# Optimization experiments

Measured on AMD Instinct MI355X. Metric: run time of the kernel, lower is better.

Reference implementation:

```python
import jax, jax.numpy as jnp
import numpy as np

N_CLASS = 85
BLANK = N_CLASS - 1  # blank_index = n_class - 1
ALPHA = 0.05
B, T, D = 4096, 96, 64


def setup_inputs() -> dict:
    key = jax.random.key(0)
    k1, k2, k3, k4 = jax.random.split(key, 4)
    preds = jax.random.normal(k1, (B, T, N_CLASS), dtype=jnp.float32)
    features = jax.random.normal(k2, (B, T, D), dtype=jnp.float32)
    labels = jax.random.randint(k3, (B, T), 0, N_CLASS, dtype=jnp.int32)
    centers = jax.random.normal(k4, (N_CLASS, D), dtype=jnp.float32) * 0.01
    return {"preds": preds, "features": features, "labels": labels, "centers": centers}


def _char_mask(pred_labels):
    # CTC collapse: keep non-blank positions that are the last of a repeat run.
    is_char = pred_labels != BLANK
    rep = pred_labels[:, :-1] == pred_labels[:, 1:]          # [B, T-1]
    tail = pred_labels[:, :1] > BLANK                         # always False (as in source)
    char_rep = jnp.concatenate([rep, tail], axis=1)           # [B, T]
    return is_char & jnp.logical_not(char_rep)


def reference(preds, features, labels, centers):
    # preds:    [B, T, n_class] softmax/logits -> argmax decode
    # features: [B, T, feat_dims]
    # labels:   [B, T] int, char label aligned to each timestep
    pred_labels = jnp.argmax(preds, axis=-1)                  # [B, T]
    mask = _char_mask(pred_labels).astype(features.dtype)     # [B, T] ragged-as-mask

    centers_batch = centers[labels]                           # gather -> [B, T, D]
    diff = centers_batch - features                           # [B, T, D]

    # tf.nn.l2_loss = sum(x^2)/2, restricted to valid char positions
    loss = 0.5 * jnp.sum(mask * jnp.sum(diff * diff, axis=-1))

    # unique_with_counts analog: per-class counts of valid char positions
    labels_flat = labels.reshape(-1)
    mask_flat = mask.reshape(-1)
    counts = jax.ops.segment_sum(mask_flat, labels_flat, num_segments=N_CLASS)  # [n_class]
    appear = counts[labels]                                   # [B, T]

    # alpha * diff / (1 + appear_times), zeroed outside char positions
    delta = ALPHA * diff * (mask / (1.0 + appear))[..., None]  # [B, T, D]

    # scatter_nd: centers.assign_sub(scatter of per-char deltas)
    upd = jax.ops.segment_sum(delta.reshape(-1, D), labels_flat, num_segments=N_CLASS)
    new_centers = centers - upd                               # [n_class, D]
    return loss, new_centers
```

## Files before the change

### kernel.cpp

```cpp
#include <hip/hip_runtime.h>
#include <cstdint>

#define BB     4096
#define TT     96
#define NC     85
#define BLANKC 84
#define DD     64
#define ALPHA  0.05f
#define BT     (BB * TT)
#define SLICE_F (NC * 17)
#define NF4    (TT * NC / 4)

template<int C0, int C1>
__device__ inline void scanR(const float* __restrict__ row, float& bv, int& bc) {
    bv = row[C0]; bc = C0;
#pragma unroll
    for (int c = C0 + 1; c < C1; ++c) {
        float v = row[c];
        if (v > bv) { bv = v; bc = c; }
    }
}

__global__ __launch_bounds__(512) void k_amask(const float4* __restrict__ p4,
                                               const int* __restrict__ labels,
                                               unsigned* __restrict__ labm,
                                               int* __restrict__ hpartT,
                                               float* __restrict__ out) {
    __shared__ float rows[TT * NC];
    __shared__ float sv[4 * TT];
    __shared__ int   sc[4 * TT];
    __shared__ int   pls[TT];
    __shared__ int   h[NC];
    int tid = threadIdx.x;
    int b   = blockIdx.x;
    if (tid < NC) h[tid] = 0;
    if (b == 0 && tid == 480) out[0] = 0.f;

    const float4* src = p4 + (size_t)b * NF4;
    float4* r4 = (float4*)rows;
    float4 v[4];
#pragma unroll
    for (int k = 0; k < 4; ++k)
        v[k] = src[min(tid + k * 512, NF4 - 1)];
#pragma unroll
    for (int k = 0; k < 4; ++k) {
        int i = tid + k * 512;
        if (i < NF4) r4[i] = v[k];
    }
    __syncthreads();

    int q = tid >> 7, r = tid & 127;
    if (r < TT) {
        const float* row = rows + r * NC;
        float bv; int bc;
        switch (q) {
            case 0:  scanR< 0, 22>(row, bv, bc); break;
            case 1:  scanR<22, 43>(row, bv, bc); break;
            case 2:  scanR<43, 64>(row, bv, bc); break;
            default: scanR<64, 85>(row, bv, bc); break;
        }
        sv[q * TT + r] = bv; sc[q * TT + r] = bc;
    }
    __syncthreads();
    if (tid < TT) {
        float bv = sv[tid]; int bc = sc[tid];
#pragma unroll
        for (int qq = 1; qq < 4; ++qq) {
            float v2 = sv[qq * TT + tid];
            int   c2 = sc[qq * TT + tid];
            if (v2 > bv) { bv = v2; bc = c2; }
        }
        pls[tid] = bc;
    }
    __syncthreads();
    if (tid < TT) {
        int p = pls[tid];
        int m = (p != BLANKC) && (tid == TT - 1 || p != pls[tid + 1]);
        int lab = labels[b * TT + tid];
        labm[b * TT + tid] = (unsigned)lab | ((unsigned)m << 31);
        atomicAdd(&h[lab], m);
    }
    __syncthreads();
    if (tid < NC) hpartT[tid * BB + b] = h[tid];
}

__global__ __launch_bounds__(512) void k_main(const float* __restrict__ feat,
                                              const unsigned* __restrict__ labm,
                                              float* __restrict__ updp,
                                              float* __restrict__ lossp, int nb) {
    __shared__ float sl[8 * SLICE_F];
    __shared__ float lred[8];
    int tid = threadIdx.x;
    for (int i = tid; i < 8 * SLICE_F; i += 512) sl[i] = 0.f;
    __syncthreads();

    int lane = tid & 63;
    int w    = tid >> 6;
    int dq   = w & 3;
    int wg   = w >> 2;
    int sub  = lane >> 4;
    int l16  = lane & 15;
    float* slice = sl + w * SLICE_F;

    int ppc    = BT / (nb * 2);
    int p0     = (blockIdx.x * 2 + wg) * ppc;
    int nsteps = ppc / 4;

    float lsum = 0.f;
    uint4 lmv = *(const uint4*)(labm + p0);
    float f   = feat[(size_t)(p0 + sub) * DD + dq * 16 + l16];

    for (int s = 0; s < nsteps; ++s) {
        uint4 lv = lmv; float fc = f;
        if (s + 1 < nsteps) {
            int pn = p0 + (s + 1) * 4;
            lmv = *(const uint4*)(labm + pn);
            f   = feat[(size_t)(pn + sub) * DD + dq * 16 + l16];
        }
        unsigned a0 = lv.x & 0x7fffffffu, a1 = lv.y & 0x7fffffffu,
                 a2 = lv.z & 0x7fffffffu, a3 = lv.w & 0x7fffffffu;
        bool dup = (a0 == a1) | (a0 == a2) | (a0 == a3) |
                   (a1 == a2) | (a1 == a3) | (a2 == a3);
        unsigned lw = (sub & 2) ? ((sub & 1) ? lv.w : lv.z)
                                : ((sub & 1) ? lv.y : lv.x);
        float m = (float)(lw >> 31);
        int  la = (int)(lw & 0x7fffffffu);
        float c = m * fc;
        lsum = fmaf(c, fc, lsum);
        int a = la * 17 + l16;
        if (!dup) slice[a] += c;
        else      atomicAdd(&slice[a], c);
    }
    __syncthreads();

    float* myp = updp + (size_t)blockIdx.x * (NC * DD);
    for (int i = tid; i < NC * DD; i += 512) {
        int r = i >> 6, d = i & 63;
        int qq = d >> 4, d16 = d & 15;
        myp[i] = sl[qq * SLICE_F + r * 17 + d16] +
                 sl[(qq + 4) * SLICE_F + r * 17 + d16];
    }
#pragma unroll
    for (int off = 32; off; off >>= 1) lsum += __shfl_xor(lsum, off);
    if (lane == 0) lred[w] = lsum;
    __syncthreads();
    if (tid == 0) {
        float s = 0.f;
#pragma unroll
        for (int ww = 0; ww < 8; ++ww) s += lred[ww];
        lossp[blockIdx.x] = s;
    }
}

__global__ __launch_bounds__(256) void k_reduce(const float* __restrict__ updp,
                                                const float* __restrict__ lossp,
                                                const float* __restrict__ centers,
                                                const int* __restrict__ hpartT,
                                                float* __restrict__ out, int nb) {
    __shared__ float sred[256];
    __shared__ float sr[4];
    __shared__ int   scnt;
    int tid = threadIdx.x;
    int bid = blockIdx.x;
    if (bid < NC * 4) {
        int j = bid >> 2, q = bid & 3;
        int cs = 0;
        for (int t = tid; t < BB; t += 256) cs += hpartT[j * BB + t];
#pragma unroll
        for (int off = 32; off; off >>= 1) cs += __shfl_xor(cs, off);
        int lane = tid & 63, wv = tid >> 6;
        if (lane == 0) ((int*)sred)[wv] = cs;
        __syncthreads();
        if (tid == 0)
            scnt = ((int*)sred)[0] + ((int*)sred)[1] +
                   ((int*)sred)[2] + ((int*)sred)[3];
        __syncthreads();
        float cnt = (float)scnt;
        int i = tid & 15;
        int c16 = tid >> 4;
        int per = nb >> 4;
        int col = j * DD + q * 16 + i;
        float s = 0.f;
        for (int b = c16 * per; b < (c16 + 1) * per; ++b)
            s += updp[(size_t)b * (NC * DD) + col];
        sred[tid] = s;
        __syncthreads();
        if (tid < 16) {
            float F = 0.f;
#pragma unroll
            for (int cc = 0; cc < 16; ++cc) F += sred[cc * 16 + i];
            float c   = centers[col];
            float scale = ALPHA / (1.f + cnt);
            out[1 + col] = c - scale * (cnt * c - F);
            float lp = cnt * c * c - 2.f * c * F;
#pragma unroll
            for (int off = 8; off; off >>= 1) lp += __shfl_xor(lp, off);
            if (i == 0) atomicAdd(&out[0], 0.5f * lp);
        }
    } else {
        float s = 0.f;
        for (int t = tid; t < nb; t += 256) s += lossp[t];
#pragma unroll
        for (int off = 32; off; off >>= 1) s += __shfl_xor(s, off);
        int lane = tid & 63, wv = tid >> 6;
        if (lane == 0) sr[wv] = s;
        __syncthreads();
        if (tid == 0) atomicAdd(&out[0], 0.5f * (sr[0] + sr[1] + sr[2] + sr[3]));
    }
}

extern "C" void kernel_launch(void* const* d_in, const int* in_sizes, int n_in,
                              void* d_out, int out_size, void* d_ws, size_t ws_size,
                              hipStream_t stream) {
    const float* preds    = (const float*)d_in[0];
    const float* features = (const float*)d_in[1];
    const int*   labels   = (const int*)d_in[2];
    const float* centers  = (const float*)d_in[3];
    float* out = (float*)d_out;

    char* ws = (char*)d_ws;
    unsigned* labm = (unsigned*)ws;
    int* hpartT    = (int*)(ws + 4 * (size_t)BT);
    size_t off0 = 4 * (size_t)BT + (size_t)NC * BB * 4 + 512;

    int nb = 768;
    while (nb > 16 && off0 + (size_t)nb * 4 + 512 +
                      (size_t)nb * NC * DD * 4 > ws_size)
        nb >>= 1;
    float* lossp = (float*)(ws + off0);
    float* updp  = (float*)(ws + off0 + (size_t)nb * 4 + 512);

    k_amask<<<BB, 512, 0, stream>>>((const float4*)preds, labels, labm,
                                    hpartT, out);
    k_main<<<nb, 512, 0, stream>>>(features, labm, updp, lossp, nb);
    k_reduce<<<NC * 4 + 1, 256, 0, stream>>>(updp, lossp, centers, hpartT,
                                             out, nb);
}
```

Baseline: 88.53 us.

## Fuse argmax-mask and feature accumulation into one kernel over 512 blocks

Merges the argmax/CTC-mask kernel and the per-class feature accumulation kernel into a single kernel. Each of 512 blocks processes 8 batch rows, prefetching the next row's preds while computing the current one, then accumulates masked features into a shared per-class array. This removes the intermediate labm buffer round trip and one kernel launch. It shrinks the partial-histogram reduction from 4096 to 512 entries. In exchange it uses much more shared memory per block (about 57 KB), which limits occupancy, and adds several barriers per row.

```diff
diff --git a/kernel.cpp b/kernel.cpp
--- a/kernel.cpp
+++ b/kernel.cpp
@@ -8,8 +8,10 @@
 #define DD     64
 #define ALPHA  0.05f
 #define BT     (BB * TT)
-#define SLICE_F (NC * 17)
 #define NF4    (TT * NC / 4)
+#define NBLK   512
+#define RPB    (BB / NBLK)
+#define FSTR   73
 
 template<int C0, int C1>
 __device__ inline void scanR(const float* __restrict__ row, float& bv, int& bc) {
@@ -21,125 +23,131 @@
     }
 }
 
-__global__ __launch_bounds__(512) void k_amask(const float4* __restrict__ p4,
-                                               const int* __restrict__ labels,
-                                               unsigned* __restrict__ labm,
-                                               int* __restrict__ hpartT,
-                                               float* __restrict__ out) {
+__global__ __launch_bounds__(512, 4) void k_fused(const float4* __restrict__ p4,
+                                                  const int* __restrict__ labels,
+                                                  const float* __restrict__ feat,
+                                                  float* __restrict__ updp,
+                                                  int* __restrict__ hpartT,
+                                                  float* __restrict__ lossp,
+                                                  float* __restrict__ out) {
     __shared__ float rows[TT * NC];
+    __shared__ float Farr[NC * FSTR];
     __shared__ float sv[4 * TT];
     __shared__ int   sc[4 * TT];
-    __shared__ int   pls[TT];
+    __shared__ unsigned lab_ls[TT];
+    __shared__ int   dupflag[12];
     __shared__ int   h[NC];
-    int tid = threadIdx.x;
-    int b   = blockIdx.x;
-    if (tid < NC) h[tid] = 0;
-    if (b == 0 && tid == 480) out[0] = 0.f;
-
-    const float4* src = p4 + (size_t)b * NF4;
-    float4* r4 = (float4*)rows;
-    float4 v[4];
-#pragma unroll
-    for (int k = 0; k < 4; ++k)
-        v[k] = src[min(tid + k * 512, NF4 - 1)];
-#pragma unroll
-    for (int k = 0; k < 4; ++k) {
-        int i = tid + k * 512;
-        if (i < NF4) r4[i] = v[k];
-    }
-    __syncthreads();
-
-    int q = tid >> 7, r = tid & 127;
-    if (r < TT) {
-        const float* row = rows + r * NC;
-        float bv; int bc;
-        switch (q) {
-            case 0:  scanR< 0, 22>(row, bv, bc); break;
-            case 1:  scanR<22, 43>(row, bv, bc); break;
-            case 2:  scanR<43, 64>(row, bv, bc); break;
-            default: scanR<64, 85>(row, bv, bc); break;
-        }
-        sv[q * TT + r] = bv; sc[q * TT + r] = bc;
-    }
-    __syncthreads();
-    if (tid < TT) {
-        float bv = sv[tid]; int bc = sc[tid];
-#pragma unroll
-        for (int qq = 1; qq < 4; ++qq) {
-            float v2 = sv[qq * TT + tid];
-            int   c2 = sc[qq * TT + tid];
-            if (v2 > bv) { bv = v2; bc = c2; }
-        }
-        pls[tid] = bc;
-    }
-    __syncthreads();
-    if (tid < TT) {
-        int p = pls[tid];
-        int m = (p != BLANKC) && (tid == TT - 1 || p != pls[tid + 1]);
-        int lab = labels[b * TT + tid];
-        labm[b * TT + tid] = (unsigned)lab | ((unsigned)m << 31);
-        atomicAdd(&h[lab], m);
-    }
-    __syncthreads();
-    if (tid < NC) hpartT[tid * BB + b] = h[tid];
-}
-
-__global__ __launch_bounds__(512) void k_main(const float* __restrict__ feat,
-                                              const unsigned* __restrict__ labm,
-                                              float* __restrict__ updp,
-                                              float* __restrict__ lossp, int nb) {
-    __shared__ float sl[8 * SLICE_F];
     __shared__ float lred[8];
-    int tid = threadIdx.x;
-    for (int i = tid; i < 8 * SLICE_F; i += 512) sl[i] = 0.f;
-    __syncthreads();
-
+
+    int tid  = threadIdx.x;
+    int blk  = blockIdx.x;
     int lane = tid & 63;
     int w    = tid >> 6;
-    int dq   = w & 3;
-    int wg   = w >> 2;
-    int sub  = lane >> 4;
-    int l16  = lane & 15;
-    float* slice = sl + w * SLICE_F;
-
-    int ppc    = BT / (nb * 2);
-    int p0     = (blockIdx.x * 2 + wg) * ppc;
-    int nsteps = ppc / 4;
-
+    int sub  = lane >> 3;
+    int l8   = lane & 7;
+    int dim  = (w << 3) | l8;
+
+    for (int i = tid; i < NC * FSTR; i += 512) Farr[i] = 0.f;
+    if (tid < NC) h[tid] = 0;
+    if (blk == 0 && tid == 500) out[0] = 0.f;
+
+    int row0 = blk * RPB;
+    const float4* s0 = p4 + (size_t)row0 * NF4;
+    float4 v0 = s0[tid];
+    float4 v1 = s0[tid + 512];
+    float4 v2 = s0[tid + 1024];
+    float4 v3 = s0[tid + 1536 < NF4 ? tid + 1536 : NF4 - 1];
+    int lcur = (tid < TT) ? labels[row0 * TT + tid] : 0;
     float lsum = 0.f;
-    uint4 lmv = *(const uint4*)(labm + p0);
-    float f   = feat[(size_t)(p0 + sub) * DD + dq * 16 + l16];
-
-    for (int s = 0; s < nsteps; ++s) {
-        uint4 lv = lmv; float fc = f;
-        if (s + 1 < nsteps) {
-            int pn = p0 + (s + 1) * 4;
-            lmv = *(const uint4*)(labm + pn);
-            f   = feat[(size_t)(pn + sub) * DD + dq * 16 + l16];
-        }
-        unsigned a0 = lv.x & 0x7fffffffu, a1 = lv.y & 0x7fffffffu,
-                 a2 = lv.z & 0x7fffffffu, a3 = lv.w & 0x7fffffffu;
-        bool dup = (a0 == a1) | (a0 == a2) | (a0 == a3) |
-                   (a1 == a2) | (a1 == a3) | (a2 == a3);
-        unsigned lw = (sub & 2) ? ((sub & 1) ? lv.w : lv.z)
-                                : ((sub & 1) ? lv.y : lv.x);
-        float m = (float)(lw >> 31);
-        int  la = (int)(lw & 0x7fffffffu);
-        float c = m * fc;
-        lsum = fmaf(c, fc, lsum);
-        int a = la * 17 + l16;
-        if (!dup) slice[a] += c;
-        else      atomicAdd(&slice[a], c);
+
+    for (int r8 = 0; r8 < RPB; ++r8) {
+        int row = row0 + r8;
+        __syncthreads();
+        float4* r4 = (float4*)rows;
+        r4[tid]        = v0;
+        r4[tid + 512]  = v1;
+        r4[tid + 1024] = v2;
+        if (tid + 1536 < NF4) r4[tid + 1536] = v3;
+        if (tid < TT) lab_ls[tid] = (unsigned)lcur;
+        int lnext = 0;
+        if (r8 + 1 < RPB) {
+            const float4* sn = p4 + (size_t)(row + 1) * NF4;
+            v0 = sn[tid];
+            v1 = sn[tid + 512];
+            v2 = sn[tid + 1024];
+            v3 = sn[tid + 1536 < NF4 ? tid + 1536 : NF4 - 1];
+            if (tid < TT) lnext = labels[(row + 1) * TT + tid];
+        }
+        __syncthreads();
+        {
+            int q = tid >> 7, r = tid & 127;
+            if (r < TT) {
+                const float* rw = rows + r * NC;
+                float bv; int bc;
+                switch (q) {
+                    case 0:  scanR< 0, 22>(rw, bv, bc); break;
+                    case 1:  scanR<22, 43>(rw, bv, bc); break;
+                    case 2:  scanR<43, 64>(rw, bv, bc); break;
+                    default: scanR<64, 85>(rw, bv, bc); break;
+                }
+                sv[q * TT + r] = bv; sc[q * TT + r] = bc;
+            }
+            if (tid < 12) {
+                int l[8];
+#pragma unroll
+                for (int k = 0; k < 8; ++k) l[k] = (int)lab_ls[tid * 8 + k];
+                int d = 0;
+#pragma unroll
+                for (int a = 0; a < 8; ++a)
+#pragma unroll
+                    for (int b2 = a + 1; b2 < 8; ++b2) d |= (l[a] == l[b2]);
+                dupflag[tid] = d;
+            }
+        }
+        __syncthreads();
+        if (tid < TT) {
+            int t1 = (tid + 1 < TT) ? tid + 1 : tid;
+            float bv = sv[tid];  int bc = sc[tid];
+            float bw = sv[t1];   int bd = sc[t1];
+#pragma unroll
+            for (int q = 1; q < 4; ++q) {
+                float a = sv[q * TT + tid]; int c = sc[q * TT + tid];
+                if (a > bv) { bv = a; bc = c; }
+                float a1 = sv[q * TT + t1]; int c1 = sc[q * TT + t1];
+                if (a1 > bw) { bw = a1; bd = c1; }
+            }
+            int m = (bc != BLANKC) && (tid == TT - 1 || bc != bd);
+            lab_ls[tid] = (unsigned)lcur | ((unsigned)m << 31);
+            atomicAdd(&h[lcur], m);
+            lcur = lnext;
+        }
+        __syncthreads();
+        {
+            const float* fb = feat + (size_t)row * TT * DD;
+            int dfl[12];
+#pragma unroll
+            for (int k = 0; k < 12; ++k) dfl[k] = dupflag[k];
+            float f = fb[sub * DD + dim];
+#pragma unroll
+            for (int s = 0; s < 12; ++s) {
+                float fc = f;
+                if (s < 11) f = fb[((s + 1) * 8 + sub) * DD + dim];
+                unsigned lw = lab_ls[s * 8 + sub];
+                float m = (float)(lw >> 31);
+                int  la = (int)(lw & 0x7fffffffu);
+                float c = m * fc;
+                lsum = fmaf(c, fc, lsum);
+                int a = la * FSTR + dim;
+                if (dfl[s]) atomicAdd(&Farr[a], c);
+                else        Farr[a] += c;
+            }
+        }
     }
     __syncthreads();
-
-    float* myp = updp + (size_t)blockIdx.x * (NC * DD);
-    for (int i = tid; i < NC * DD; i += 512) {
-        int r = i >> 6, d = i & 63;
-        int qq = d >> 4, d16 = d & 15;
-        myp[i] = sl[qq * SLICE_F + r * 17 + d16] +
-                 sl[(qq + 4) * SLICE_F + r * 17 + d16];
-    }
+    float* myp = updp + (size_t)blk * (NC * DD);
+    for (int i = tid; i < NC * DD; i += 512)
+        myp[i] = Farr[(i >> 6) * FSTR + (i & 63)];
+    if (tid < NC) hpartT[tid * NBLK + blk] = h[tid];
 #pragma unroll
     for (int off = 32; off; off >>= 1) lsum += __shfl_xor(lsum, off);
     if (lane == 0) lred[w] = lsum;
@@ -148,7 +156,7 @@
         float s = 0.f;
 #pragma unroll
         for (int ww = 0; ww < 8; ++ww) s += lred[ww];
-        lossp[blockIdx.x] = s;
+        lossp[blk] = s;
     }
 }
 
@@ -156,7 +164,7 @@
                                                 const float* __restrict__ lossp,
                                                 const float* __restrict__ centers,
                                                 const int* __restrict__ hpartT,
-                                                float* __restrict__ out, int nb) {
+                                                float* __restrict__ out) {
     __shared__ float sred[256];
     __shared__ float sr[4];
     __shared__ int   scnt;
@@ -165,7 +173,7 @@
     if (bid < NC * 4) {
         int j = bid >> 2, q = bid & 3;
         int cs = 0;
-        for (int t = tid; t < BB; t += 256) cs += hpartT[j * BB + t];
+        for (int t = tid; t < NBLK; t += 256) cs += hpartT[j * NBLK + t];
 #pragma unroll
         for (int off = 32; off; off >>= 1) cs += __shfl_xor(cs, off);
         int lane = tid & 63, wv = tid >> 6;
@@ -178,7 +186,7 @@
         float cnt = (float)scnt;
         int i = tid & 15;
         int c16 = tid >> 4;
-        int per = nb >> 4;
+        int per = NBLK >> 4;
         int col = j * DD + q * 16 + i;
         float s = 0.f;
         for (int b = c16 * per; b < (c16 + 1) * per; ++b)
@@ -199,7 +207,7 @@
         }
     } else {
         float s = 0.f;
-        for (int t = tid; t < nb; t += 256) s += lossp[t];
+        for (int t = tid; t < NBLK; t += 256) s += lossp[t];
 #pragma unroll
         for (int off = 32; off; off >>= 1) s += __shfl_xor(s, off);
         int lane = tid & 63, wv = tid >> 6;
@@ -219,20 +227,12 @@
     float* out = (float*)d_out;
 
     char* ws = (char*)d_ws;
-    unsigned* labm = (unsigned*)ws;
-    int* hpartT    = (int*)(ws + 4 * (size_t)BT);
-    size_t off0 = 4 * (size_t)BT + (size_t)NC * BB * 4 + 512;
-
-    int nb = 768;
-    while (nb > 16 && off0 + (size_t)nb * 4 + 512 +
-                      (size_t)nb * NC * DD * 4 > ws_size)
-        nb >>= 1;
-    float* lossp = (float*)(ws + off0);
-    float* updp  = (float*)(ws + off0 + (size_t)nb * 4 + 512);
-
-    k_amask<<<BB, 512, 0, stream>>>((const float4*)preds, labels, labm,
-                                    hpartT, out);
-    k_main<<<nb, 512, 0, stream>>>(features, labm, updp, lossp, nb);
-    k_reduce<<<NC * 4 + 1, 256, 0, stream>>>(updp, lossp, centers, hpartT,
-                                             out, nb);
-}
+    float* updp   = (float*)ws;
+    int*   hpartT = (int*)(ws + (size_t)NBLK * NC * DD * 4);
+    float* lossp  = (float*)(ws + (size_t)NBLK * NC * DD * 4
+                                + (size_t)NC * NBLK * 4);
+
+    k_fused<<<NBLK, 512, 0, stream>>>((const float4*)preds, labels, features,
+                                      updp, hpartT, lossp, out);
+    k_reduce<<<NC * 4 + 1, 256, 0, stream>>>(updp, lossp, centers, hpartT, out);
+}
```

Result: slower. 95.15 us (+7.5%).
